# Kernel optimization log

Hardware: AMD Instinct MI355X
Metric: run time of the kernel (lower is better)

Reference implementation:

```python
import jax, jax.numpy as jnp
import numpy as np
from jax.scipy.special import logsumexp

B, T, V, E, H, K = 64, 512, 21128, 256, 512, 31


def setup_inputs() -> dict:
    key = jax.random.key(0)
    ks = jax.random.split(key, 32)
    s = 1.0 / np.sqrt(H)

    def u(k, shape):
        return jax.random.uniform(k, shape, jnp.float32, -s, s)

    inp = {
        "input_ids": jax.random.randint(ks[0], (B, T), 0, V),
        "labels": jax.random.randint(ks[1], (B, T), 0, K),
        "emb": jax.random.normal(ks[2], (V, E), jnp.float32) * 0.05,
    }
    i = 3
    for layer, insz in (("l0", E), ("l1", 2 * H)):
        for d in ("f", "b"):
            inp["w_ih_%s%s" % (layer, d)] = u(ks[i], (3 * H, insz)); i += 1
            inp["w_hh_%s%s" % (layer, d)] = u(ks[i], (3 * H, H)); i += 1
            inp["b_ih_%s%s" % (layer, d)] = u(ks[i], (3 * H,)); i += 1
            inp["b_hh_%s%s" % (layer, d)] = u(ks[i], (3 * H,)); i += 1
    inp["cls_w"] = u(ks[i], (K, 2 * H))
    inp["cls_b"] = u(ks[i + 1], (K,))
    inp["crf_start"] = jax.random.normal(ks[i + 2], (K,), jnp.float32) * 0.1
    inp["crf_end"] = jax.random.normal(ks[i + 3], (K,), jnp.float32) * 0.1
    inp["crf_trans"] = jax.random.normal(ks[i + 4], (K, K), jnp.float32) * 0.1
    return inp


def gru_dir(x, w_ih, w_hh, b_ih, b_hh, reverse):
    # x: [B, T, in]. PyTorch GRU gate math, gates ordered (r, z, n).
    xp = jnp.einsum('bti,gi->btg', x, w_ih) + b_ih  # [B, T, 3H] precomputed input gates
    if reverse:
        xp = xp[:, ::-1]
    h0 = jnp.zeros((x.shape[0], w_hh.shape[1]), x.dtype)

    def step(h, xt):
        gh = h @ w_hh.T + b_hh
        xr, xz, xn = jnp.split(xt, 3, axis=-1)
        hr, hz, hn = jnp.split(gh, 3, axis=-1)
        r = jax.nn.sigmoid(xr + hr)
        z = jax.nn.sigmoid(xz + hz)
        n = jnp.tanh(xn + r * hn)
        h_new = (1.0 - z) * n + z * h
        return h_new, h_new

    _, hs = jax.lax.scan(step, h0, jnp.swapaxes(xp, 0, 1))
    hs = jnp.swapaxes(hs, 0, 1)  # [B, T, H]
    if reverse:
        hs = hs[:, ::-1]
    return hs


def crf_llh(emissions, tags, mask, start, end, trans):
    # Linear-chain CRF log-likelihood, summed over batch. mask[:, 0] assumed True.
    Bn = emissions.shape[0]
    mf = mask.astype(emissions.dtype)
    bidx = jnp.arange(Bn)
    em_t = jnp.take_along_axis(emissions, tags[:, :, None], axis=2)[:, :, 0]  # [B, T]
    num = start[tags[:, 0]] + em_t[:, 0]
    tr = trans[tags[:, :-1], tags[:, 1:]]  # [B, T-1]
    num = num + jnp.sum((tr + em_t[:, 1:]) * mf[:, 1:], axis=1)
    last_idx = jnp.sum(mask.astype(jnp.int32), axis=1) - 1
    num = num + end[tags[bidx, last_idx]]

    alpha0 = start[None, :] + emissions[:, 0]  # [B, K]

    def step(alpha, inp):
        em, m = inp  # em [B, K], m [B]
        nxt = logsumexp(alpha[:, :, None] + trans[None] + em[:, None, :], axis=1)
        return jnp.where(m[:, None], nxt, alpha), None

    alpha, _ = jax.lax.scan(
        step, alpha0,
        (jnp.swapaxes(emissions[:, 1:], 0, 1), jnp.swapaxes(mask[:, 1:], 0, 1)))
    denom = logsumexp(alpha + end[None, :], axis=1)
    return jnp.sum(num - denom)


def reference(input_ids, labels, emb,
              w_ih_l0f, w_hh_l0f, b_ih_l0f, b_hh_l0f,
              w_ih_l0b, w_hh_l0b, b_ih_l0b, b_hh_l0b,
              w_ih_l1f, w_hh_l1f, b_ih_l1f, b_hh_l1f,
              w_ih_l1b, w_hh_l1b, b_ih_l1b, b_hh_l1b,
              cls_w, cls_b, crf_start, crf_end, crf_trans):
    x = emb[input_ids]  # [B, T, E]
    f0 = gru_dir(x, w_ih_l0f, w_hh_l0f, b_ih_l0f, b_hh_l0f, False)
    b0 = gru_dir(x, w_ih_l0b, w_hh_l0b, b_ih_l0b, b_hh_l0b, True)
    h1 = jnp.concatenate([f0, b0], axis=-1)  # [B, T, 2H]
    f1 = gru_dir(h1, w_ih_l1f, w_hh_l1f, b_ih_l1f, b_hh_l1f, False)
    b1 = gru_dir(h1, w_ih_l1b, w_hh_l1b, b_ih_l1b, b_hh_l1b, True)
    gru_out = jnp.concatenate([f1, b1], axis=-1)  # [B, T, 2H]
    emissions = jnp.einsum('bth,kh->btk', gru_out, cls_w) + cls_b  # [B, T, K]
    mask = labels > -1  # labels.gt(labels_padding_value=-1)
    loss = -crf_llh(emissions, labels, mask, crf_start, crf_end, crf_trans)
    return (loss, emissions)
```

## Files before the change

kernel.cpp:

```cpp
#include <hip/hip_runtime.h>

#define DI __device__ __forceinline__

constexpr int B_  = 64;
constexpr int T_  = 512;
constexpr int E_  = 256;
constexpr int H_  = 512;
constexpr int G_  = 1536;
constexpr int H2_ = 1024;
constexpr int K_  = 31;
constexpr int BT_ = B_ * T_;
constexpr int TC_ = 64;
constexpr int NC_ = T_ / TC_;

typedef float        f32x4  __attribute__((ext_vector_type(4)));
typedef short        bf16x8 __attribute__((ext_vector_type(8)));
typedef unsigned int u32x4  __attribute__((ext_vector_type(4)));
typedef unsigned long long ull;

DI float bf2f(unsigned short u) {
    union { unsigned int i; float f; } v; v.i = ((unsigned int)u) << 16; return v.f;
}
DI unsigned short f2bf(float f) {
    union { float f; unsigned int i; } v; v.f = f;
    unsigned int r = v.i + 0x7fffu + ((v.i >> 16) & 1u);
    return (unsigned short)(r >> 16);
}
DI float sigm(float x) { return 1.f / (1.f + __expf(-x)); }
DI float tanh_(float x) {
    x = fminf(15.f, fmaxf(-15.f, x));
    float e = __expf(-2.f * x);
    return (1.f - e) / (1.f + e);
}

#define MFMA16(a, b, c) __builtin_amdgcn_mfma_f32_16x16x32_bf16(a, b, c, 0, 0, 0)

__global__ __launch_bounds__(256) void cvt_cls(const float* __restrict__ src,
                                               unsigned short* __restrict__ dstf,
                                               unsigned short* __restrict__ dstb) {
    int i = blockIdx.x * 256 + threadIdx.x;
    if (i >= 32 * H_) return;
    int n = i >> 9, k = i & 511;
    float vf = (n < K_) ? src[n * H2_ + k] : 0.f;
    float vb = (n < K_) ? src[n * H2_ + H_ + k] : 0.f;
    dstf[i] = f2bf(vf);
    dstb[i] = f2bf(vb);
}

__global__ __launch_bounds__(256) void emis_bias_init(const float* __restrict__ cls_b,
                                                      float* __restrict__ out1) {
    int i = blockIdx.x * 256 + threadIdx.x;
    int stride = gridDim.x * 256;
    for (; i < BT_ * K_; i += stride) {
        int n = i - (i / K_) * K_;
        out1[i] = cls_b[n];
    }
}

template <bool OUTF32, bool ACCUM, bool WF32, bool AGATHER>
DI void gemm_tile(unsigned short (*As)[40], unsigned short (*Ws)[40],
                  const unsigned short* A, const float* gsrc, const int* ids, int lda,
                  size_t arow0, const void* W, int ldw, int nrows, int n0,
                  const float* bias, void* Cout, int ldc, size_t crow0,
                  int nout, int ksz, int tid) {
    const int w = tid >> 6, l = tid & 63;
    const int srow = tid >> 2, sc8 = (tid & 3) * 8;
    const int mw = (w >> 1) * 32, nw = (w & 1) * 32;
    const int fl = l & 15, fk = (l >> 4) * 8;
    f32x4 z4 = { 0.f, 0.f, 0.f, 0.f };
    f32x4 acc[2][2];
    acc[0][0] = z4; acc[0][1] = z4; acc[1][0] = z4; acc[1][1] = z4;
    size_t abase;
    if (AGATHER) abase = (size_t)ids[arow0 + srow] * lda;
    else         abase = (arow0 + srow) * (size_t)lda;

    for (int kc = 0; kc < ksz; kc += 32) {
        u32x4 av, wvv;
        if (AGATHER) {
            const float4* ap = (const float4*)(gsrc + abase + kc + sc8);
            float4 a0 = ap[0], a1 = ap[1];
            union { unsigned short s[8]; u32x4 v; } r;
            r.s[0] = f2bf(a0.x); r.s[1] = f2bf(a0.y); r.s[2] = f2bf(a0.z); r.s[3] = f2bf(a0.w);
            r.s[4] = f2bf(a1.x); r.s[5] = f2bf(a1.y); r.s[6] = f2bf(a1.z); r.s[7] = f2bf(a1.w);
            av = r.v;
        } else {
            av = *(const u32x4*)(A + abase + kc + sc8);
        }
        if (WF32) {
            const float4* wp = (const float4*)((const float*)W + (size_t)(n0 + srow) * ldw + kc + sc8);
            float4 w0 = wp[0], w1 = wp[1];
            union { unsigned short s[8]; u32x4 v; } r;
            r.s[0] = f2bf(w0.x); r.s[1] = f2bf(w0.y); r.s[2] = f2bf(w0.z); r.s[3] = f2bf(w0.w);
            r.s[4] = f2bf(w1.x); r.s[5] = f2bf(w1.y); r.s[6] = f2bf(w1.z); r.s[7] = f2bf(w1.w);
            wvv = r.v;
        } else {
            if (n0 + srow < nrows)
                wvv = *(const u32x4*)((const unsigned short*)W + (size_t)(n0 + srow) * ldw + kc + sc8);
            else { u32x4 zz = { 0u, 0u, 0u, 0u }; wvv = zz; }
        }
        __syncthreads();
        *(u32x4*)&As[srow][sc8] = av;
        *(u32x4*)&Ws[srow][sc8] = wvv;
        __syncthreads();
        bf16x8 a0 = *(const bf16x8*)&As[mw + fl][fk];
        bf16x8 a1 = *(const bf16x8*)&As[mw + 16 + fl][fk];
        bf16x8 b0 = *(const bf16x8*)&Ws[nw + fl][fk];
        bf16x8 b1 = *(const bf16x8*)&Ws[nw + 16 + fl][fk];
        acc[0][0] = MFMA16(a0, b0, acc[0][0]);
        acc[0][1] = MFMA16(a0, b1, acc[0][1]);
        acc[1][0] = MFMA16(a1, b0, acc[1][0]);
        acc[1][1] = MFMA16(a1, b1, acc[1][1]);
    }

    #pragma unroll
    for (int mf = 0; mf < 2; ++mf)
        #pragma unroll
        for (int nf = 0; nf < 2; ++nf) {
            int col = n0 + nw + nf * 16 + fl;
            if (col >= nout) continue;
            float bv = bias ? bias[col] : 0.f;
            #pragma unroll
            for (int j = 0; j < 4; ++j) {
                int r = mw + mf * 16 + (l >> 4) * 4 + j;
                size_t crow = crow0 + r;
                float v = acc[mf][nf][j] + bv;
                if (OUTF32) {
                    float* C = (float*)Cout;
                    if (ACCUM) C[crow * ldc + col] += v;
                    else       C[crow * ldc + col] = v;
                } else {
                    ((unsigned short*)Cout)[crow * ldc + col] = f2bf(v);
                }
            }
        }
}

template <bool OUTF32, bool ACCUM, bool WF32, bool AGATHER>
__global__ __launch_bounds__(256) void gemm_k(
        const unsigned short* __restrict__ A, const float* __restrict__ gsrc,
        const int* __restrict__ ids, int lda, int m_base, int astride,
        const void* __restrict__ W, int ldw, int nrows,
        const float* __restrict__ bias,
        void* __restrict__ Cout, int ldc, int c_base, int cstride, int nout, int ksz) {
    __shared__ unsigned short As[64][40];
    __shared__ unsigned short Ws[64][40];
    gemm_tile<OUTF32, ACCUM, WF32, AGATHER>(As, Ws, A, gsrc, ids, lda,
        (size_t)m_base + (size_t)blockIdx.x * astride, W, ldw, nrows,
        blockIdx.y * 64, bias, Cout, ldc,
        (size_t)c_base + (size_t)blockIdx.x * cstride, nout, ksz, threadIdx.x);
}

template <bool AGATHER>
__global__ __launch_bounds__(256, 1) void fused_scan_gemm(
        int c, int layer,
        const unsigned short* __restrict__ xpc_f, const unsigned short* __restrict__ xpc_b,
        const float* __restrict__ whh_f, const float* __restrict__ whh_b,
        const float* __restrict__ bhh_f, const float* __restrict__ bhh_b,
        unsigned int* __restrict__ hpub,
        float* __restrict__ hcar,
        unsigned short* __restrict__ out_f, unsigned short* __restrict__ out_b,
        int ldo, int mode, int* __restrict__ flags,
        const unsigned short* __restrict__ gA, const float* __restrict__ gsrc,
        const int* __restrict__ gids, int glda,
        const float* __restrict__ gwf, const float* __restrict__ gwb,
        const float* __restrict__ gbf, const float* __restrict__ gbb,
        unsigned short* __restrict__ xpf_nxt, unsigned short* __restrict__ xpb_nxt,
        int t0f_n, int t0b_n, int do_gemm) {
    __shared__ unsigned short As[64][40];
    __shared__ unsigned short Ws[64][40];
    __shared__ unsigned short hs[16 * 512];
    const int bid = blockIdx.x;
    const int tid = threadIdx.x;

    if (bid >= 64) {
        if (!do_gemm) return;
        const int gb = bid - 64;
        for (int job = gb; job < 2 * 64 * 24; job += 192) {
            int dirj = job & 1;
            int rest = job >> 1;
            int mt = rest & 63;
            int nt = rest >> 6;
            const float* gw = dirj ? gwb : gwf;
            const float* gbias = dirj ? gbb : gbf;
            unsigned short* gout = dirj ? xpb_nxt : xpf_nxt;
            int t0 = dirj ? t0b_n : t0f_n;
            gemm_tile<false, false, true, AGATHER>(As, Ws, gA, gsrc, gids, glda,
                (size_t)t0 + (size_t)mt * T_, gw, glda, G_, nt * 64, gbias,
                (void*)gout, G_, (size_t)mt * TC_, G_, glda, tid);
        }
        return;
    }

    const int dir = bid >> 5;
    const int rb  = bid & 31;
    const int ug  = rb >> 2;
    const int bg  = rb & 3;
    const int w = tid >> 6, l = tid & 63;
    const int fl = l & 15, q = l >> 4, fko = q * 8;
    const unsigned short* xp = dir ? xpc_b : xpc_f;
    const float* whh = dir ? whh_b : whh_f;
    const float* bhh = dir ? bhh_b : bhh_f;
    unsigned short* outp = dir ? out_b : out_f;
    int* pollb  = flags + (dir * 4 + bg) * 8 * 32;
    int* myflag = pollb + ug * 32;

    const int u0w = ug * 64 + w * 16;
    bf16x8 wv[3][16];
    #pragma unroll
    for (int g = 0; g < 3; ++g)
        #pragma unroll
        for (int ks = 0; ks < 16; ++ks) {
            const float* wp = whh + (size_t)(g * H_ + u0w + fl) * H_ + ks * 32 + fko;
            float4 w0 = *(const float4*)wp, w1 = *(const float4*)(wp + 4);
            union { unsigned short s[8]; bf16x8 v; } r;
            r.s[0] = f2bf(w0.x); r.s[1] = f2bf(w0.y); r.s[2] = f2bf(w0.z); r.s[3] = f2bf(w0.w);
            r.s[4] = f2bf(w1.x); r.s[5] = f2bf(w1.y); r.s[6] = f2bf(w1.z); r.s[7] = f2bf(w1.w);
            wv[g][ks] = r.v;
        }

    const int u = u0w + fl;
    const float br_ = bhh[u], bz_ = bhh[H_ + u], bn_ = bhh[2 * H_ + u];
    const int mb = bg * 16 + q * 4;
    const int srowl = tid >> 4;
    const int sseg  = tid & 15;

    float hp[4];
    if (c > 0) {
        #pragma unroll
        for (int j = 0; j < 4; ++j) hp[j] = hcar[dir * (B_ * H_) + (mb + j) * H_ + u];
    } else {
        #pragma unroll
        for (int j = 0; j < 4; ++j) hp[j] = 0.f;
    }

    unsigned short xg[3][4];
    auto ldxp = [&](int tl) {
        #pragma unroll
        for (int j = 0; j < 4; ++j) {
            const unsigned short* xb = xp + ((size_t)((mb + j) * TC_ + tl) * G_) + u;
            xg[0][j] = xb[0]; xg[1][j] = xb[H_]; xg[2][j] = xb[2 * H_];
        }
    };
    ldxp(dir ? (TC_ - 1) : 0);

    for (int sl = 0; sl < TC_; ++sl) {
        const int s  = c * TC_ + sl;
        const int gs = layer * T_ + s;
        const int t = dir ? (T_ - 1 - s) : s;
        const int tloc = dir ? (TC_ - 1 - sl) : sl;

        f32x4 z4 = { 0.f, 0.f, 0.f, 0.f };
        f32x4 acc[3];
        acc[0] = z4; acc[1] = z4; acc[2] = z4;

        if (s > 0) {
            if (sl > 0) {
                int v = gs;
                if (l < 8) v = __hip_atomic_load(pollb + l * 32, __ATOMIC_RELAXED, __HIP_MEMORY_SCOPE_AGENT);
                while (!__all(v >= gs)) {
                    __builtin_amdgcn_s_sleep(1);
                    if (l < 8) v = __hip_atomic_load(pollb + l * 32, __ATOMIC_RELAXED, __HIP_MEMORY_SCOPE_AGENT);
                }
                asm volatile("" ::: "memory");
            }
            {
                const ull* src = (const ull*)(hpub
                    + ((size_t)((((s - 1) & 1) * 2 + dir) * B_ + bg * 16 + srowl)) * 256)
                    + sseg * 8;
                ull qv[8];
                #pragma unroll
                for (int i = 0; i < 8; ++i)
                    qv[i] = __hip_atomic_load(src + i, __ATOMIC_RELAXED, __HIP_MEMORY_SCOPE_AGENT);
                char* dst = (char*)hs + srowl * 1024;
                #pragma unroll
                for (int i = 0; i < 4; ++i) {
                    unsigned int byt = (unsigned int)(sseg * 64 + i * 16);
                    byt ^= ((unsigned int)(srowl & 7)) << 4;
                    union { ull qq[2]; u32x4 v4; } pk;
                    pk.qq[0] = qv[2 * i]; pk.qq[1] = qv[2 * i + 1];
                    *(u32x4*)(dst + byt) = pk.v4;
                }
            }
            __syncthreads();
            #pragma unroll
            for (int ks = 0; ks < 16; ++ks) {
                unsigned int byt = (unsigned int)(ks * 64 + q * 16);
                byt ^= ((unsigned int)(fl & 7)) << 4;
                bf16x8 afr = *(const bf16x8*)((const char*)hs + fl * 1024 + byt);
                acc[0] = MFMA16(afr, wv[0][ks], acc[0]);
                acc[1] = MFMA16(afr, wv[1][ks], acc[1]);
                acc[2] = MFMA16(afr, wv[2][ks], acc[2]);
            }
        }

        unsigned short hb16s[4];
        #pragma unroll
        for (int j = 0; j < 4; ++j) {
            float xr = bf2f(xg[0][j]);
            float xz = bf2f(xg[1][j]);
            float xn = bf2f(xg[2][j]);
            float r = sigm(xr + acc[0][j] + br_);
            float z = sigm(xz + acc[1][j] + bz_);
            float nn = tanh_(xn + r * (acc[2][j] + bn_));
            float hv = (1.f - z) * nn + z * hp[j];
            hp[j] = hv;
            hb16s[j] = f2bf(hv);
        }

        unsigned int* hw = hpub + (size_t)((s & 1) * 2 + dir) * (B_ * 256);
        #pragma unroll
        for (int j = 0; j < 4; ++j) {
            unsigned int pv = (unsigned int)(unsigned short)__shfl_xor((int)hb16s[j], 1);
            if ((fl & 1) == 0) {
                unsigned int pk32 = (unsigned int)hb16s[j] | (pv << 16);
                __hip_atomic_store(hw + (size_t)(mb + j) * 256 + (u >> 1), pk32,
                                   __ATOMIC_RELAXED, __HIP_MEMORY_SCOPE_AGENT);
            }
        }
        asm volatile("s_waitcnt vmcnt(0)" ::: "memory");
        __syncthreads();
        if (tid == 0)
            __hip_atomic_store(myflag, gs + 1, __ATOMIC_RELAXED, __HIP_MEMORY_SCOPE_AGENT);

        #pragma unroll
        for (int j = 0; j < 4; ++j) {
            size_t row = mode ? (size_t)((mb + j) * TC_ + tloc) : ((size_t)(mb + j) * T_ + t);
            outp[row * ldo + u] = hb16s[j];
        }
        if (sl < TC_ - 1) ldxp(dir ? (TC_ - 2 - sl) : (sl + 1));
    }

    #pragma unroll
    for (int j = 0; j < 4; ++j) hcar[dir * (B_ * H_) + (mb + j) * H_ + u] = hp[j];
}

__global__ __launch_bounds__(64) void crf_kernel(const float* __restrict__ em,
                                                 const int* __restrict__ labels,
                                                 const float* __restrict__ start,
                                                 const float* __restrict__ endv,
                                                 const float* __restrict__ trans,
                                                 float* __restrict__ partials) {
    __shared__ float tr[32 * 32];
    const int b = blockIdx.x, l = threadIdx.x;
    for (int e2 = l; e2 < 961; e2 += 64) {
        int r = e2 / 31, cc = e2 - r * 31;
        tr[r * 32 + cc] = trans[e2];
    }
    if (l < 32) tr[31 * 32 + l] = 0.f;
    __syncthreads();
    const int* lab = labels + b * T_;
    const float* eb = em + (size_t)b * T_ * K_;

    float part = 0.f, cnt = 0.f;
    for (int t = l; t < T_; t += 64) {
        int lt = lab[t];
        if (lt > -1) {
            cnt += 1.f;
            if (t > 0) part += tr[lab[t - 1] * 32 + lt] + eb[t * K_ + lt];
        }
    }
    #pragma unroll
    for (int o = 32; o; o >>= 1) { part += __shfl_xor(part, o); cnt += __shfl_xor(cnt, o); }
    int lastidx = (int)cnt - 1;
    float num = part + start[lab[0]] + eb[lab[0]] + endv[lab[lastidx]];

    const int jj = l & 31, half = l >> 5;
    const int i0 = half * 16;
    const int ecol = (jj < K_) ? jj : (K_ - 1);
    float a = (jj < K_) ? (start[jj] + eb[jj]) : -3.0e38f;
    for (int t = 1; t < T_; ++t) {
        float tv[16];
        float m = -3.0e38f;
        #pragma unroll
        for (int k = 0; k < 16; ++k) {
            float av = __shfl(a, i0 + k);
            float x = av + tr[(i0 + k) * 32 + jj];
            tv[k] = x;
            m = fmaxf(m, x);
        }
        float ss = 0.f;
        #pragma unroll
        for (int k = 0; k < 16; ++k) ss += __expf(tv[k] - m);
        float m2 = __shfl_xor(m, 32), s2 = __shfl_xor(ss, 32);
        float M = fmaxf(m, m2);
        float S = ss * __expf(m - M) + s2 * __expf(m2 - M);
        float anew = eb[t * K_ + ecol] + M + __logf(S);
        a = ((lab[t] > -1) && (jj < K_)) ? anew : a;
    }
    float v = (jj < K_) ? (a + endv[jj]) : -3.0e38f;
    float m = v;
    #pragma unroll
    for (int o = 32; o; o >>= 1) m = fmaxf(m, __shfl_xor(m, o));
    float ss = (half == 0 && jj < K_) ? __expf(v - m) : 0.f;
    #pragma unroll
    for (int o = 32; o; o >>= 1) ss += __shfl_xor(ss, o);
    if (l == 0) partials[b] = num - (m + __logf(ss));
}

__global__ __launch_bounds__(64) void loss_reduce(const float* __restrict__ partials,
                                                  float* __restrict__ out) {
    float v = partials[threadIdx.x];
    #pragma unroll
    for (int o = 32; o; o >>= 1) v += __shfl_xor(v, o);
    if (threadIdx.x == 0) out[0] = -v;
}

__global__ void sentinel(float* __restrict__ out, float v) { out[0] = -v; }

extern "C" void kernel_launch(void* const* d_in, const int* in_sizes, int n_in,
                              void* d_out, int out_size, void* d_ws, size_t ws_size,
                              hipStream_t stream) {
    const int*   ids      = (const int*)d_in[0];
    const int*   labels   = (const int*)d_in[1];
    const float* emb      = (const float*)d_in[2];
    const float* wih[4]   = { (const float*)d_in[3], (const float*)d_in[7], (const float*)d_in[11], (const float*)d_in[15] };
    const float* whh[4]   = { (const float*)d_in[4], (const float*)d_in[8], (const float*)d_in[12], (const float*)d_in[16] };
    const float* bih[4]   = { (const float*)d_in[5], (const float*)d_in[9], (const float*)d_in[13], (const float*)d_in[17] };
    const float* bhh[4]   = { (const float*)d_in[6], (const float*)d_in[10], (const float*)d_in[14], (const float*)d_in[18] };
    const float* cls_w    = (const float*)d_in[19];
    const float* cls_b    = (const float*)d_in[20];
    const float* c_start  = (const float*)d_in[21];
    const float* c_end    = (const float*)d_in[22];
    const float* c_trans  = (const float*)d_in[23];
    float* out = (float*)d_out;
    float* out1 = out + 1;

    char* p = (char*)d_ws;
    size_t used = 0;
    auto alloc = [&](size_t bytes) -> char* {
        char* r = p;
        size_t a = (bytes + 255) & ~(size_t)255;
        p += a; used += a;
        return r;
    };
    unsigned short* xpF[2]; unsigned short* xpB[2];
    for (int i = 0; i < 2; ++i) {
        xpF[i] = (unsigned short*)alloc((size_t)B_ * TC_ * G_ * 2);
        xpB[i] = (unsigned short*)alloc((size_t)B_ * TC_ * G_ * 2);
    }
    unsigned short* h1   = (unsigned short*)alloc((size_t)BT_ * H2_ * 2);
    unsigned short* gof  = (unsigned short*)alloc((size_t)B_ * TC_ * H_ * 2);
    unsigned short* gob  = (unsigned short*)alloc((size_t)B_ * TC_ * H_ * 2);
    unsigned short* clsf  = (unsigned short*)alloc((size_t)32 * H_ * 2);
    unsigned short* clshb = (unsigned short*)alloc((size_t)32 * H_ * 2);
    unsigned int*   hpub  = (unsigned int*)alloc((size_t)2 * 2 * B_ * 256 * 4);
    float*          hcar  = (float*)alloc((size_t)2 * B_ * H_ * 4);
    float*          partials = (float*)alloc((size_t)B_ * 4);
    int*            flags = (int*)alloc((size_t)2 * 4 * 8 * 32 * 4);

    if (used > ws_size) {
        sentinel<<<dim3(1), dim3(1), 0, stream>>>(out, (float)(ws_size >> 20));
        return;
    }

    hipMemsetAsync(flags, 0, (size_t)2 * 4 * 8 * 32 * 4, stream);
    cvt_cls<<<dim3((32 * H_ + 255) / 256), dim3(256), 0, stream>>>(cls_w, clsf, clshb);
    emis_bias_init<<<dim3(1024), dim3(256), 0, stream>>>(cls_b, out1);

    for (int layer = 0; layer < 2; ++layer) {
        const float* wf  = wih[layer * 2 + 0];
        const float* wb  = wih[layer * 2 + 1];
        const float* bf_ = bih[layer * 2 + 0];
        const float* bb_ = bih[layer * 2 + 1];
        const float* whf = whh[layer * 2 + 0];
        const float* whb = whh[layer * 2 + 1];
        const float* bhf = bhh[layer * 2 + 0];
        const float* bhb = bhh[layer * 2 + 1];

        if (layer == 0) {
            gemm_k<false, false, true, true><<<dim3(64, 24), dim3(256), 0, stream>>>(
                nullptr, emb, ids, E_, 0, T_, wf, E_, G_, bf_, (void*)xpF[0], G_, 0, TC_, G_, E_);
            gemm_k<false, false, true, true><<<dim3(64, 24), dim3(256), 0, stream>>>(
                nullptr, emb, ids, E_, T_ - TC_, T_, wb, E_, G_, bb_, (void*)xpB[0], G_, 0, TC_, G_, E_);
        } else {
            gemm_k<false, false, true, false><<<dim3(64, 24), dim3(256), 0, stream>>>(
                h1, nullptr, nullptr, H2_, 0, T_, wf, H2_, G_, bf_, (void*)xpF[0], G_, 0, TC_, G_, H2_);
            gemm_k<false, false, true, false><<<dim3(64, 24), dim3(256), 0, stream>>>(
                h1, nullptr, nullptr, H2_, T_ - TC_, T_, wb, H2_, G_, bb_, (void*)xpB[0], G_, 0, TC_, G_, H2_);
        }

        for (int c = 0; c < NC_; ++c) {
            int dg = (c + 1 < NC_) ? 1 : 0;
            int t0f_n = (c + 1) * TC_;
            int t0b_n = T_ - (c + 2) * TC_;
            if (layer == 0) {
                fused_scan_gemm<true><<<dim3(256), dim3(256), 0, stream>>>(
                    c, 0, xpF[c & 1], xpB[c & 1], whf, whb, bhf, bhb, hpub, hcar,
                    h1, h1 + H_, H2_, 0, flags,
                    nullptr, emb, ids, E_, wf, wb, bf_, bb_,
                    xpF[(c + 1) & 1], xpB[(c + 1) & 1], t0f_n, t0b_n, dg);
            } else {
                fused_scan_gemm<false><<<dim3(256), dim3(256), 0, stream>>>(
                    c, 1, xpF[c & 1], xpB[c & 1], whf, whb, bhf, bhb, hpub, hcar,
                    gof, gob, H_, 1, flags,
                    h1, nullptr, nullptr, H2_, wf, wb, bf_, bb_,
                    xpF[(c + 1) & 1], xpB[(c + 1) & 1], t0f_n, t0b_n, dg);
                int t0f = c * TC_;
                int t0b = T_ - (c + 1) * TC_;
                gemm_k<true, true, false, false><<<dim3(64, 1), dim3(256), 0, stream>>>(
                    gof, nullptr, nullptr, H_, 0, TC_, clsf, H_, 32, nullptr,
                    (void*)out1, K_, t0f, T_, K_, H_);
                gemm_k<true, true, false, false><<<dim3(64, 1), dim3(256), 0, stream>>>(
                    gob, nullptr, nullptr, H_, 0, TC_, clshb, H_, 32, nullptr,
                    (void*)out1, K_, t0b, T_, K_, H_);
            }
        }
    }

    crf_kernel<<<dim3(B_), dim3(64), 0, stream>>>(out1, labels, c_start, c_end, c_trans, partials);
    loss_reduce<<<dim3(1), dim3(64), 0, stream>>>(partials, out);
}
```

Before: 4.572 ms.

## Pre-convert W_hh to bf16, relax per-step wait, merge emission GEMMs

W_hh is converted to bf16 once per layer by a separate kernel, so each chunk launch of the scan kernel loads bf16 weights directly instead of converting fp32 on every launch. The per-step flag publish now follows the output store and next-step xp prefetch, with a partial vmcnt wait and a raw s_barrier, so those memory ops overlap the cross-block handoff. The two emission GEMM launches per chunk are merged into one 2-D launch. The partial vmcnt(16) wait relies on in-order counter retirement to guarantee the hpub stores are visible before the flag, which is fragile if instruction counts change.

Result: faster. 4.322 ms (-5.5%).

```diff
diff --git a/kernel.cpp b/kernel.cpp
--- a/kernel.cpp
+++ b/kernel.cpp
@@ -34,6 +34,12 @@
 }
 
 #define MFMA16(a, b, c) __builtin_amdgcn_mfma_f32_16x16x32_bf16(a, b, c, 0, 0, 0)
+
+__global__ void cvt_f32_bf16(const float* __restrict__ src, unsigned short* __restrict__ dst, int n) {
+    int i = blockIdx.x * blockDim.x + threadIdx.x;
+    int stride = gridDim.x * blockDim.x;
+    for (; i < n; i += stride) dst[i] = f2bf(src[i]);
+}
 
 __global__ __launch_bounds__(256) void cvt_cls(const float* __restrict__ src,
                                                unsigned short* __restrict__ dstf,
@@ -150,11 +156,25 @@
         (size_t)c_base + (size_t)blockIdx.x * cstride, nout, ksz, threadIdx.x);
 }
 
+__global__ __launch_bounds__(256) void emis_k(
+        const unsigned short* __restrict__ gof, const unsigned short* __restrict__ gob,
+        const unsigned short* __restrict__ clsf, const unsigned short* __restrict__ clsb,
+        float* __restrict__ out1, int t0f, int t0b) {
+    __shared__ unsigned short As[64][40];
+    __shared__ unsigned short Ws[64][40];
+    const unsigned short* A = blockIdx.y ? gob : gof;
+    const unsigned short* W = blockIdx.y ? clsb : clsf;
+    int t0 = blockIdx.y ? t0b : t0f;
+    gemm_tile<true, true, false, false>(As, Ws, A, nullptr, nullptr, H_,
+        (size_t)blockIdx.x * TC_, W, H_, 32, 0, nullptr,
+        (void*)out1, K_, (size_t)t0 + (size_t)blockIdx.x * T_, K_, H_, threadIdx.x);
+}
+
 template <bool AGATHER>
 __global__ __launch_bounds__(256, 1) void fused_scan_gemm(
         int c, int layer,
         const unsigned short* __restrict__ xpc_f, const unsigned short* __restrict__ xpc_b,
-        const float* __restrict__ whh_f, const float* __restrict__ whh_b,
+        const unsigned short* __restrict__ whh_f, const unsigned short* __restrict__ whh_b,
         const float* __restrict__ bhh_f, const float* __restrict__ bhh_b,
         unsigned int* __restrict__ hpub,
         float* __restrict__ hcar,
@@ -198,7 +218,7 @@
     const int w = tid >> 6, l = tid & 63;
     const int fl = l & 15, q = l >> 4, fko = q * 8;
     const unsigned short* xp = dir ? xpc_b : xpc_f;
-    const float* whh = dir ? whh_b : whh_f;
+    const unsigned short* whh = dir ? whh_b : whh_f;
     const float* bhh = dir ? bhh_b : bhh_f;
     unsigned short* outp = dir ? out_b : out_f;
     int* pollb  = flags + (dir * 4 + bg) * 8 * 32;
@@ -209,14 +229,8 @@
     #pragma unroll
     for (int g = 0; g < 3; ++g)
         #pragma unroll
-        for (int ks = 0; ks < 16; ++ks) {
-            const float* wp = whh + (size_t)(g * H_ + u0w + fl) * H_ + ks * 32 + fko;
-            float4 w0 = *(const float4*)wp, w1 = *(const float4*)(wp + 4);
-            union { unsigned short s[8]; bf16x8 v; } r;
-            r.s[0] = f2bf(w0.x); r.s[1] = f2bf(w0.y); r.s[2] = f2bf(w0.z); r.s[3] = f2bf(w0.w);
-            r.s[4] = f2bf(w1.x); r.s[5] = f2bf(w1.y); r.s[6] = f2bf(w1.z); r.s[7] = f2bf(w1.w);
-            wv[g][ks] = r.v;
-        }
+        for (int ks = 0; ks < 16; ++ks)
+            wv[g][ks] = *(const bf16x8*)(whh + (size_t)(g * H_ + u0w + fl) * H_ + ks * 32 + fko);
 
     const int u = u0w + fl;
     const float br_ = bhh[u], bz_ = bhh[H_ + u], bn_ = bhh[2 * H_ + u];
@@ -317,17 +331,17 @@
                                    __ATOMIC_RELAXED, __HIP_MEMORY_SCOPE_AGENT);
             }
         }
-        asm volatile("s_waitcnt vmcnt(0)" ::: "memory");
-        __syncthreads();
-        if (tid == 0)
-            __hip_atomic_store(myflag, gs + 1, __ATOMIC_RELAXED, __HIP_MEMORY_SCOPE_AGENT);
-
+        asm volatile("" ::: "memory");
         #pragma unroll
         for (int j = 0; j < 4; ++j) {
             size_t row = mode ? (size_t)((mb + j) * TC_ + tloc) : ((size_t)(mb + j) * T_ + t);
             outp[row * ldo + u] = hb16s[j];
         }
         if (sl < TC_ - 1) ldxp(dir ? (TC_ - 2 - sl) : (sl + 1));
+        asm volatile("s_waitcnt vmcnt(16)" ::: "memory");
+        __builtin_amdgcn_s_barrier();
+        if (tid == 0)
+            __hip_atomic_store(myflag, gs + 1, __ATOMIC_RELAXED, __HIP_MEMORY_SCOPE_AGENT);
     }
 
     #pragma unroll
@@ -443,6 +457,8 @@
     unsigned short* gob  = (unsigned short*)alloc((size_t)B_ * TC_ * H_ * 2);
     unsigned short* clsf  = (unsigned short*)alloc((size_t)32 * H_ * 2);
     unsigned short* clshb = (unsigned short*)alloc((size_t)32 * H_ * 2);
+    unsigned short* whhbf = (unsigned short*)alloc((size_t)G_ * H_ * 2);
+    unsigned short* whhbb = (unsigned short*)alloc((size_t)G_ * H_ * 2);
     unsigned int*   hpub  = (unsigned int*)alloc((size_t)2 * 2 * B_ * 256 * 4);
     float*          hcar  = (float*)alloc((size_t)2 * B_ * H_ * 4);
     float*          partials = (float*)alloc((size_t)B_ * 4);
@@ -462,10 +478,11 @@
         const float* wb  = wih[layer * 2 + 1];
         const float* bf_ = bih[layer * 2 + 0];
         const float* bb_ = bih[layer * 2 + 1];
-        const float* whf = whh[layer * 2 + 0];
-        const float* whb = whh[layer * 2 + 1];
         const float* bhf = bhh[layer * 2 + 0];
         const float* bhb = bhh[layer * 2 + 1];
+
+        cvt_f32_bf16<<<dim3(2048), dim3(256), 0, stream>>>(whh[layer * 2 + 0], whhbf, G_ * H_);
+        cvt_f32_bf16<<<dim3(2048), dim3(256), 0, stream>>>(whh[layer * 2 + 1], whhbb, G_ * H_);
 
         if (layer == 0) {
             gemm_k<false, false, true, true><<<dim3(64, 24), dim3(256), 0, stream>>>(
@@ -485,24 +502,19 @@
             int t0b_n = T_ - (c + 2) * TC_;
             if (layer == 0) {
                 fused_scan_gemm<true><<<dim3(256), dim3(256), 0, stream>>>(
-                    c, 0, xpF[c & 1], xpB[c & 1], whf, whb, bhf, bhb, hpub, hcar,
+                    c, 0, xpF[c & 1], xpB[c & 1], whhbf, whhbb, bhf, bhb, hpub, hcar,
                     h1, h1 + H_, H2_, 0, flags,
                     nullptr, emb, ids, E_, wf, wb, bf_, bb_,
                     xpF[(c + 1) & 1], xpB[(c + 1) & 1], t0f_n, t0b_n, dg);
             } else {
                 fused_scan_gemm<false><<<dim3(256), dim3(256), 0, stream>>>(
-                    c, 1, xpF[c & 1], xpB[c & 1], whf, whb, bhf, bhb, hpub, hcar,
+                    c, 1, xpF[c & 1], xpB[c & 1], whhbf, whhbb, bhf, bhb, hpub, hcar,
                     gof, gob, H_, 1, flags,
                     h1, nullptr, nullptr, H2_, wf, wb, bf_, bb_,
                     xpF[(c + 1) & 1], xpB[(c + 1) & 1], t0f_n, t0b_n, dg);
                 int t0f = c * TC_;
                 int t0b = T_ - (c + 1) * TC_;
-                gemm_k<true, true, false, false><<<dim3(64, 1), dim3(256), 0, stream>>>(
-                    gof, nullptr, nullptr, H_, 0, TC_, clsf, H_, 32, nullptr,
-                    (void*)out1, K_, t0f, T_, K_, H_);
-                gemm_k<true, true, false, false><<<dim3(64, 1), dim3(256), 0, stream>>>(
-                    gob, nullptr, nullptr, H_, 0, TC_, clshb, H_, 32, nullptr,
-                    (void*)out1, K_, t0b, T_, K_, H_);
+                emis_k<<<dim3(64, 2), dim3(256), 0, stream>>>(gof, gob, clsf, clshb, out1, t0f, t0b);
             }
         }
     }
```
